# Kernel optimization log

Measured on AMD Instinct MI355X. Metric: run time of the kernel, lower is better.

The kernel has to match this reference:

```python
import jax, jax.numpy as jnp
import numpy as np

NUM_HIDDEN = 256   # per-head dim == model dim in this module
NUM_HEADS = 8
SEQ_LEN = 2048
BATCH = 4
D_K = 256          # self.d_k used for the softmax scale


def setup_inputs() -> dict:
    key = jax.random.key(0)
    ks = jax.random.split(key, 12)
    H, D = NUM_HEADS, NUM_HIDDEN
    init = lambda k, shape: (jax.random.normal(k, shape, dtype=jnp.float32) * 0.02)
    return {
        "query": jax.random.normal(ks[0], (BATCH, SEQ_LEN, D), dtype=jnp.float32),
        "key": jax.random.normal(ks[1], (BATCH, SEQ_LEN, D), dtype=jnp.float32),
        "values": jax.random.normal(ks[2], (BATCH, SEQ_LEN, D), dtype=jnp.float32),
        "Wq": init(ks[3], (H * D, D)), "bq": init(ks[4], (H * D,)),
        "Wk": init(ks[5], (H * D, D)), "bk": init(ks[6], (H * D,)),
        "Wv": init(ks[7], (H * D, D)), "bv": init(ks[8], (H * D,)),
        "Wo": init(ks[9], (D, H * D)), "bo": init(ks[10], (D,)),
    }


def reference(query, key, values, Wq, bq, Wk, bk, Wv, bv, Wo, bo):
    B, S, D = query.shape
    H = Wq.shape[0] // D
    # Linear projections to [B, S, H*D], then the module's raw reshape to [B, H, S, D]
    # (note: this is a plain view, NOT the usual split-heads transpose -> faithful to source)
    q = (jnp.einsum("bsd,ed->bse", query, Wq) + bq).reshape(B, H, S, D)
    k = (jnp.einsum("bsd,ed->bse", key, Wk) + bk).reshape(B, H, S, D)
    v = (jnp.einsum("bsd,ed->bse", values, Wv) + bv).reshape(B, H, S, D)
    # scores: [B, H, S, S], scaled by sqrt(d_k); default path applies no mask
    scores = jnp.einsum("bhqd,bhkd->bhqk", q, k) / jnp.sqrt(jnp.float32(D_K))
    attn = jax.nn.softmax(scores, axis=-1)
    # dropout in eval mode: identity
    out = jnp.einsum("bhqk,bhkd->bhqd", attn, v)            # [B, H, S, D]
    out = out.transpose(0, 2, 1, 3).reshape(B, S, H * D)    # [B, S, H*D]
    return jnp.einsum("bse,de->bsd", out, Wo) + bo          # [B, S, D]
```

## Files before the change

### kernel.cpp

```cpp
#include <hip/hip_runtime.h>
#include <hip/hip_bf16.h>
#include <stdint.h>

#define B_SZ 4
#define H_N 8
#define S_LEN 2048
#define D_HEAD 256
#define HD 2048

typedef __attribute__((ext_vector_type(8))) short bf16x8;
typedef __attribute__((ext_vector_type(4))) float f32x4;
typedef __attribute__((ext_vector_type(4))) uint32_t u32x4;
typedef __hip_bfloat16 bf16;

typedef __attribute__((address_space(1))) const void glob_cv;
typedef __attribute__((address_space(3))) void lds_v;

__device__ __forceinline__ short f2bf(float f) {
  bf16 h = __float2bfloat16(f);
  return *reinterpret_cast<short*>(&h);
}

__device__ __forceinline__ uint32_t cvtpk(float lo, float hi) {
  uint32_t r;
  asm volatile("v_cvt_pk_bf16_f32 %0, %1, %2" : "=v"(r) : "v"(lo), "v"(hi));
  return r;
}

__global__ __launch_bounds__(256) void cvt_all(
    const float* __restrict__ w0, bf16* __restrict__ o0,
    const float* __restrict__ w1, bf16* __restrict__ o1,
    const float* __restrict__ w2, bf16* __restrict__ o2,
    const float* __restrict__ w3, bf16* __restrict__ o3,
    const float* __restrict__ x0, bf16* __restrict__ y0,
    const float* __restrict__ x1, bf16* __restrict__ y1,
    const float* __restrict__ x2, bf16* __restrict__ y2) {
  int bid = blockIdx.x;
  const float* src; bf16* dst; int off;
  if (bid < 1024) {
    int k = bid >> 8; off = (bid & 255) * 2048;
    src = k == 0 ? w0 : k == 1 ? w1 : k == 2 ? w2 : w3;
    dst = k == 0 ? o0 : k == 1 ? o1 : k == 2 ? o2 : o3;
  } else {
    int j = bid - 1024; int k = j >> 10; off = (j & 1023) * 2048;
    src = k == 0 ? x0 : k == 1 ? x1 : x2;
    dst = k == 0 ? y0 : k == 1 ? y1 : y2;
  }
  int i = off + threadIdx.x * 8;
  float4 a = *(const float4*)(src + i);
  float4 b = *(const float4*)(src + i + 4);
  bf16x8 o;
  o[0] = f2bf(a.x); o[1] = f2bf(a.y); o[2] = f2bf(a.z); o[3] = f2bf(a.w);
  o[4] = f2bf(b.x); o[5] = f2bf(b.y); o[6] = f2bf(b.z); o[7] = f2bf(b.w);
  *reinterpret_cast<bf16x8*>(dst + i) = o;
}

__global__ __launch_bounds__(256, 2) void proj3(
    const bf16* __restrict__ A0, const bf16* __restrict__ A1, const bf16* __restrict__ A2,
    const bf16* __restrict__ B0, const bf16* __restrict__ B1, const bf16* __restrict__ B2,
    const float* __restrict__ c0, const float* __restrict__ c1, const float* __restrict__ c2,
    bf16* __restrict__ O0, bf16* __restrict__ O1, bf16* __restrict__ O2) {
  constexpr int HALF = 2 * 128 * 128;
  __shared__ __align__(16) char lds[2 * HALF];

  int which = blockIdx.y;
  const bf16* A = which == 0 ? A0 : which == 1 ? A1 : A2;
  const bf16* Bm = which == 0 ? B0 : which == 1 ? B1 : B2;
  const float* bias = which == 0 ? c0 : which == 1 ? c1 : c2;
  bf16* OutP = which == 0 ? O0 : which == 1 ? O1 : O2;
  float scale = which == 0 ? (1.0f / 16.0f) * 1.44269504f : 1.0f;

  int tid = threadIdx.x;
  int w = tid >> 6, l = tid & 63;
  int l15 = l & 15, lg = l >> 4;
  int wr = w >> 1, wc = w & 1;

  int bid = blockIdx.x;
  int wg = (bid & 7) * 128 + (bid >> 3);
  int mt = wg >> 4, nt = wg & 15;
  int m0 = mt * 128, n0 = nt * 128;

  const size_t K2 = 512;
  char* ldsp = (char*)lds;
  const char* Abase = (const char*)A + (size_t)m0 * K2;
  const char* Bbase = (const char*)Bm + (size_t)n0 * K2;

  auto ISSUE = [&](int buf, int kt) {
    const char* As = Abase + (size_t)kt * 128;
    const char* Bs = Bbase + (size_t)kt * 128;
    char* db = ldsp + buf * HALF;
#pragma unroll
    for (int i = 0; i < 4; ++i) {
      int c = tid + i * 256, row = c >> 3;
      __builtin_amdgcn_global_load_lds((glob_cv*)(As + (size_t)row * K2 + 16 * ((c & 7) ^ (row & 7))),
                                       (lds_v*)(db + c * 16), 16, 0, 0);
    }
#pragma unroll
    for (int i = 0; i < 4; ++i) {
      int c = tid + i * 256, row = c >> 3;
      __builtin_amdgcn_global_load_lds((glob_cv*)(Bs + (size_t)row * K2 + 16 * ((c & 7) ^ (row & 7))),
                                       (lds_v*)(db + 16384 + c * 16), 16, 0, 0);
    }
  };

  f32x4 acc[4][4];
#pragma unroll
  for (int mi = 0; mi < 4; ++mi)
#pragma unroll
    for (int ni = 0; ni < 4; ++ni) acc[mi][ni] = f32x4{0.f, 0.f, 0.f, 0.f};

  ISSUE(0, 0);
  for (int kt = 0; kt < 4; ++kt) {
    int cur = kt & 1;
    if (kt < 3) {
      ISSUE(cur ^ 1, kt + 1);
      asm volatile("s_waitcnt vmcnt(8)" ::: "memory");
    } else {
      asm volatile("s_waitcnt vmcnt(0)" ::: "memory");
    }
    __builtin_amdgcn_s_barrier();
    __builtin_amdgcn_sched_barrier(0);

    const char* bufc = ldsp + cur * HALF;
#pragma unroll
    for (int kb2 = 0; kb2 < 2; ++kb2) {
      int swz = 16 * ((kb2 * 4 + lg) ^ (l15 & 7));
      bf16x8 af[4], bfr[4];
#pragma unroll
      for (int mi = 0; mi < 4; ++mi)
        af[mi] = *(const bf16x8*)(bufc + (wr * 64 + mi * 16 + l15) * 128 + swz);
#pragma unroll
      for (int ni = 0; ni < 4; ++ni)
        bfr[ni] = *(const bf16x8*)(bufc + 16384 + (wc * 64 + ni * 16 + l15) * 128 + swz);
#pragma unroll
      for (int mi = 0; mi < 4; ++mi)
#pragma unroll
        for (int ni = 0; ni < 4; ++ni)
          acc[mi][ni] = __builtin_amdgcn_mfma_f32_16x16x32_bf16(af[mi], bfr[ni], acc[mi][ni], 0, 0, 0);
    }
    __builtin_amdgcn_sched_barrier(0);
    __builtin_amdgcn_s_barrier();
  }

  if (which == 2) {
    bf16* tp = (bf16*)lds;
#pragma unroll
    for (int ni = 0; ni < 4; ++ni) {
      int colL = wc * 64 + ni * 16 + l15;
      float bv = bias[n0 + colL];
#pragma unroll
      for (int mi = 0; mi < 4; ++mi) {
        short4 pk4;
        pk4.x = f2bf(acc[mi][ni][0] + bv);
        pk4.y = f2bf(acc[mi][ni][1] + bv);
        pk4.z = f2bf(acc[mi][ni][2] + bv);
        pk4.w = f2bf(acc[mi][ni][3] + bv);
        *(short4*)(tp + colL * 136 + wr * 64 + mi * 16 + lg * 4) = pk4;
      }
    }
    __syncthreads();
    int b = m0 >> 11, h = (m0 >> 8) & 7;
    int ehi = n0 >> 8, t0 = m0 & 255;
    bf16* vb = OutP + (size_t)(b * 8 + h) * D_HEAD * S_LEN;
#pragma unroll
    for (int p = 0; p < 8; ++p) {
      int colL = p * 16 + (tid >> 4);
      int d = (n0 & 255) + colL;
      int4 v = *(const int4*)(tp + colL * 136 + (tid & 15) * 8);
      *(int4*)(vb + (size_t)d * S_LEN + ehi * 256 + t0 + (tid & 15) * 8) = v;
    }
  } else {
#pragma unroll
    for (int ni = 0; ni < 4; ++ni) {
      int col = n0 + wc * 64 + ni * 16 + l15;
      float bv = bias[col];
#pragma unroll
      for (int mi = 0; mi < 4; ++mi) {
#pragma unroll
        for (int r = 0; r < 4; ++r) {
          float v = (acc[mi][ni][r] + bv) * scale;
          int row = m0 + wr * 64 + mi * 16 + lg * 4 + r;
          int b = row >> 11;
          int h = (row >> 8) & 7;
          int d = col & 255;
          size_t off;
          if (which == 1) {
            int jj = (col >> 8) * 256 + (row & 255);
            off = (((size_t)(b * 8 + h) * S_LEN) + jj) * D_HEAD + d;
          } else {
            int sp = ((row & 255) << 3) | (col >> 8);
            off = (((size_t)(b * 8 + h) * S_LEN) + sp) * D_HEAD + d;
          }
          OutP[off] = __float2bfloat16(v);
        }
      }
    }
  }
}

__global__ __launch_bounds__(256, 2) void out_gemm(const bf16* __restrict__ A,
                                                   const bf16* __restrict__ Bm,
                                                   const float* __restrict__ bias,
                                                   float* __restrict__ Out) {
  constexpr int HALF = 2 * 64 * 128;
  __shared__ __align__(16) char lds[2 * HALF];

  int tid = threadIdx.x;
  int w = tid >> 6, l = tid & 63;
  int l15 = l & 15, lg = l >> 4;
  int wr = w >> 1, wc = w & 1;

  int bid = blockIdx.x;
  int wg = (bid & 7) * 64 + (bid >> 3);
  int mt = wg >> 2, nt = wg & 3;
  int m0 = mt * 64, n0 = nt * 64;

  const size_t K2 = 4096;
  char* ldsp = (char*)lds;
  const char* Abase = (const char*)A + (size_t)m0 * K2;
  const char* Bbase = (const char*)Bm + (size_t)n0 * K2;

  auto ISSUE = [&](int buf, int kt) {
    const char* As = Abase + (size_t)kt * 128;
    const char* Bs = Bbase + (size_t)kt * 128;
    char* db = ldsp + buf * HALF;
#pragma unroll
    for (int i = 0; i < 2; ++i) {
      int c = tid + i * 256, row = c >> 3;
      __builtin_amdgcn_global_load_lds((glob_cv*)(As + (size_t)row * K2 + 16 * ((c & 7) ^ (row & 7))),
                                       (lds_v*)(db + c * 16), 16, 0, 0);
    }
#pragma unroll
    for (int i = 0; i < 2; ++i) {
      int c = tid + i * 256, row = c >> 3;
      __builtin_amdgcn_global_load_lds((glob_cv*)(Bs + (size_t)row * K2 + 16 * ((c & 7) ^ (row & 7))),
                                       (lds_v*)(db + 8192 + c * 16), 16, 0, 0);
    }
  };

  f32x4 acc[2][2];
#pragma unroll
  for (int mi = 0; mi < 2; ++mi)
#pragma unroll
    for (int ni = 0; ni < 2; ++ni) acc[mi][ni] = f32x4{0.f, 0.f, 0.f, 0.f};

  ISSUE(0, 0);
  for (int kt = 0; kt < 32; ++kt) {
    int cur = kt & 1;
    if (kt < 31) {
      ISSUE(cur ^ 1, kt + 1);
      asm volatile("s_waitcnt vmcnt(4)" ::: "memory");
    } else {
      asm volatile("s_waitcnt vmcnt(0)" ::: "memory");
    }
    __builtin_amdgcn_s_barrier();
    __builtin_amdgcn_sched_barrier(0);

    const char* bufc = ldsp + cur * HALF;
#pragma unroll
    for (int kb2 = 0; kb2 < 2; ++kb2) {
      int swz = 16 * ((kb2 * 4 + lg) ^ (l15 & 7));
      bf16x8 af[2], bfr[2];
#pragma unroll
      for (int mi = 0; mi < 2; ++mi)
        af[mi] = *(const bf16x8*)(bufc + (wr * 32 + mi * 16 + l15) * 128 + swz);
#pragma unroll
      for (int ni = 0; ni < 2; ++ni)
        bfr[ni] = *(const bf16x8*)(bufc + 8192 + (wc * 32 + ni * 16 + l15) * 128 + swz);
#pragma unroll
      for (int mi = 0; mi < 2; ++mi)
#pragma unroll
        for (int ni = 0; ni < 2; ++ni)
          acc[mi][ni] = __builtin_amdgcn_mfma_f32_16x16x32_bf16(af[mi], bfr[ni], acc[mi][ni], 0, 0, 0);
    }
    __builtin_amdgcn_sched_barrier(0);
    __builtin_amdgcn_s_barrier();
  }

#pragma unroll
  for (int ni = 0; ni < 2; ++ni) {
    int col = n0 + wc * 32 + ni * 16 + l15;
    float bv = bias[col];
#pragma unroll
    for (int mi = 0; mi < 2; ++mi)
#pragma unroll
      for (int r = 0; r < 4; ++r)
        Out[(size_t)(m0 + wr * 32 + mi * 16 + lg * 4 + r) * 256 + col] = acc[mi][ni][r] + bv;
  }
}

__global__ __launch_bounds__(256, 2) void attn_kernel(const bf16* __restrict__ Qp,
                                                      const bf16* __restrict__ Kp,
                                                      const bf16* __restrict__ Vt,
                                                      bf16* __restrict__ AL) {
  __shared__ __align__(16) bf16 KVs[2 * 16384];

  int tid = threadIdx.x;
  int w = tid >> 6, l = tid & 63;
  int l15 = l & 15, lg = l >> 4;
  int l31 = l & 31, hl = l >> 5;

  int bid = blockIdx.x;
  int xcd = bid & 7, j = bid >> 3;
  int bh = xcd + 8 * (j >> 4);
  int qt = j & 15;

  const bf16* Qb = Qp + (size_t)bh * S_LEN * D_HEAD;
  const bf16* Kb = Kp + (size_t)bh * S_LEN * D_HEAD;
  const bf16* Vb = Vt + (size_t)bh * (size_t)D_HEAD * S_LEN;

  int q0 = qt * 128 + w * 32;

  bf16x8 qf0[8], qf1[8];
#pragma unroll
  for (int kb = 0; kb < 8; ++kb) {
    qf0[kb] = *(const bf16x8*)(Qb + (size_t)(q0 + l15) * D_HEAD + kb * 32 + lg * 8);
    qf1[kb] = *(const bf16x8*)(Qb + (size_t)(q0 + 16 + l15) * D_HEAD + kb * 32 + lg * 8);
  }

  f32x4 acc0[16], acc1[16];
#pragma unroll
  for (int n = 0; n < 16; ++n) {
    acc0[n] = f32x4{0.f, 0.f, 0.f, 0.f};
    acc1[n] = f32x4{0.f, 0.f, 0.f, 0.f};
  }
  float lp0 = 0.f, lp1 = 0.f;

  int kvp = 2 * (l31 & 15) + (l31 >> 4);
  const char* pK = (const char*)Kb + (size_t)kvp * 512 + (size_t)(w * 256 + hl * 16);
  const char* pV = (const char*)Vb + (size_t)l * 4096 + (size_t)((w - 2) * 32);
  int dK = w * 8192 + l * 16;
  int dV = 16384 + (w - 2) * 8192 + l * 16;
  char* ldsBase = (char*)&KVs[0];

  auto ISSUE = [&](int buf) {
    char* bb = ldsBase + buf * 32768;
    if (w < 2) {
#pragma unroll
      for (int i = 0; i < 8; ++i)
        __builtin_amdgcn_global_load_lds((glob_cv*)(pK + i * 32),
                                         (lds_v*)(bb + dK + i * 1024), 16, 0, 0);
      pK += 32 * 512;
    } else {
#pragma unroll
      for (int i = 0; i < 8; ++i)
        __builtin_amdgcn_global_load_lds((glob_cv*)(pV + (i & 3) * 262144 + (i >> 2) * 16),
                                         (lds_v*)(bb + dV + (i & 3) * 1024 + (i >> 2) * 4096), 16, 0, 0);
      pV += 64;
    }
  };

  int krd = lg * 256 + l15 * 8;
  int vrd = 8192 + lg * 2048 + l15 * 8;

  ISSUE(0);

  for (int kt = 0; kt < 64; ++kt) {
    int cur = kt & 1;
    asm volatile("s_waitcnt vmcnt(0)" ::: "memory");
    __builtin_amdgcn_s_barrier();
    __builtin_amdgcn_sched_barrier(0);
    if (kt < 63) ISSUE(cur ^ 1);

    const bf16* bufp = &KVs[cur * 16384];

    f32x4 s00 = f32x4{0.f,0.f,0.f,0.f}, s01 = f32x4{0.f,0.f,0.f,0.f};
    f32x4 s10 = f32x4{0.f,0.f,0.f,0.f}, s11 = f32x4{0.f,0.f,0.f,0.f};
    __builtin_amdgcn_s_setprio(1);
#pragma unroll
    for (int kb = 0; kb < 8; ++kb) {
      bf16x8 kf0 = *(const bf16x8*)(bufp + krd + kb * 1024);
      bf16x8 kf1 = *(const bf16x8*)(bufp + krd + kb * 1024 + 128);
      s00 = __builtin_amdgcn_mfma_f32_16x16x32_bf16(kf0, qf0[kb], s00, 0, 0, 0);
      s01 = __builtin_amdgcn_mfma_f32_16x16x32_bf16(kf1, qf0[kb], s01, 0, 0, 0);
      s10 = __builtin_amdgcn_mfma_f32_16x16x32_bf16(kf0, qf1[kb], s10, 0, 0, 0);
      s11 = __builtin_amdgcn_mfma_f32_16x16x32_bf16(kf1, qf1[kb], s11, 0, 0, 0);
    }
    __builtin_amdgcn_s_setprio(0);

    float p00[4], p01[4], p10[4], p11[4];
#pragma unroll
    for (int r = 0; r < 4; ++r) {
      p00[r] = exp2f(s00[r]); p01[r] = exp2f(s01[r]);
      p10[r] = exp2f(s10[r]); p11[r] = exp2f(s11[r]);
    }
    lp0 += (p00[0] + p01[0]) + (p00[1] + p01[1]) + (p00[2] + p01[2]) + (p00[3] + p01[3]);
    lp1 += (p10[0] + p11[0]) + (p10[1] + p11[1]) + (p10[2] + p11[2]) + (p10[3] + p11[3]);

    union { u32x4 wq; bf16x8 v; } pu0, pu1;
    pu0.wq[0] = cvtpk(p00[0], p01[0]); pu0.wq[1] = cvtpk(p00[1], p01[1]);
    pu0.wq[2] = cvtpk(p00[2], p01[2]); pu0.wq[3] = cvtpk(p00[3], p01[3]);
    pu1.wq[0] = cvtpk(p10[0], p11[0]); pu1.wq[1] = cvtpk(p10[1], p11[1]);
    pu1.wq[2] = cvtpk(p10[2], p11[2]); pu1.wq[3] = cvtpk(p10[3], p11[3]);
    bf16x8 pa0 = pu0.v, pa1 = pu1.v;

    __builtin_amdgcn_s_setprio(1);
#pragma unroll
    for (int n = 0; n < 16; ++n) {
      bf16x8 vbf = *(const bf16x8*)(bufp + vrd + n * 128);
      acc0[n] = __builtin_amdgcn_mfma_f32_16x16x32_bf16(pa0, vbf, acc0[n], 0, 0, 0);
      acc1[n] = __builtin_amdgcn_mfma_f32_16x16x32_bf16(pa1, vbf, acc1[n], 0, 0, 0);
    }
    __builtin_amdgcn_s_setprio(0);
  }

  float t0 = lp0;
  t0 += __shfl_xor(t0, 16);
  t0 += __shfl_xor(t0, 32);
  float inv0 = 1.0f / t0;
  float t1 = lp1;
  t1 += __shfl_xor(t1, 16);
  t1 += __shfl_xor(t1, 32);
  float inv1 = 1.0f / t1;
  float i00 = __shfl(inv0, lg * 4 + 0), i01 = __shfl(inv0, lg * 4 + 1);
  float i02 = __shfl(inv0, lg * 4 + 2), i03 = __shfl(inv0, lg * 4 + 3);
  float i10 = __shfl(inv1, lg * 4 + 0), i11 = __shfl(inv1, lg * 4 + 1);
  float i12 = __shfl(inv1, lg * 4 + 2), i13 = __shfl(inv1, lg * 4 + 3);
  int b = bh >> 3, h = bh & 7;
#pragma unroll
  for (int r = 0; r < 4; ++r) {
    float v0 = r == 0 ? i00 : r == 1 ? i01 : r == 2 ? i02 : i03;
    float v1 = r == 0 ? i10 : r == 1 ? i11 : r == 2 ? i12 : i13;
    int qa = q0 + lg * 4 + r;
    int qb = qa + 16;
    bf16* orow0 = AL + ((size_t)b * S_LEN + qa) * HD + h * D_HEAD;
    bf16* orow1 = AL + ((size_t)b * S_LEN + qb) * HD + h * D_HEAD;
#pragma unroll
    for (int n = 0; n < 16; ++n) {
      orow0[n * 16 + l15] = __float2bfloat16(acc0[n][r] * v0);
      orow1[n * 16 + l15] = __float2bfloat16(acc1[n][r] * v1);
    }
  }
}

extern "C" void kernel_launch(void* const* d_in, const int* in_sizes, int n_in,
                              void* d_out, int out_size, void* d_ws, size_t ws_size,
                              hipStream_t stream) {
  (void)in_sizes; (void)n_in; (void)out_size; (void)ws_size;
  const float* query  = (const float*)d_in[0];
  const float* key    = (const float*)d_in[1];
  const float* values = (const float*)d_in[2];
  const float* Wq = (const float*)d_in[3];
  const float* bq = (const float*)d_in[4];
  const float* Wk = (const float*)d_in[5];
  const float* bk = (const float*)d_in[6];
  const float* Wv = (const float*)d_in[7];
  const float* bv = (const float*)d_in[8];
  const float* Wo = (const float*)d_in[9];
  const float* bo = (const float*)d_in[10];
  float* out = (float*)d_out;

  bf16* ws = (bf16*)d_ws;
  const size_t NP = (size_t)B_SZ * H_N * S_LEN * D_HEAD;
  const size_t NW = (size_t)HD * D_HEAD;
  const size_t NX = (size_t)B_SZ * S_LEN * D_HEAD;
  bf16* Qp  = ws;
  bf16* Kp  = Qp + NP;
  bf16* Vtp = Kp + NP;
  bf16* ALb = Vtp + NP;
  bf16* Wqb = ALb + NP;
  bf16* Wkb = Wqb + NW;
  bf16* Wvb = Wkb + NW;
  bf16* Wob = Wvb + NW;
  bf16* Xqb = ALb;
  bf16* Xkb = ALb + NX;
  bf16* Xvb = ALb + 2 * NX;

  cvt_all<<<4096, 256, 0, stream>>>(Wq, Wqb, Wk, Wkb, Wv, Wvb, Wo, Wob,
                                    query, Xqb, key, Xkb, values, Xvb);

  proj3<<<dim3(1024, 3), 256, 0, stream>>>(Xqb, Xkb, Xvb, Wqb, Wkb, Wvb,
                                           bq, bk, bv, Qp, Kp, Vtp);

  attn_kernel<<<512, 256, 0, stream>>>(Qp, Kp, Vtp, ALb);

  out_gemm<<<512, 256, 0, stream>>>(ALb, Wob, bo, out);
}
```

Baseline: 233.1 us.

## Software-pipeline attention loop: overlap PV of previous tile with QK of current

Restructures the attention inner loop so the P·V MFMAs for the previous key tile are issued right after the Q·K MFMAs of the current tile, and the exp/convert work follows them. The aim is to hide the softmax exp and packing latency behind matrix-core work. K stays double-buffered while V moves to a triple buffer so the previous tile's V remains valid. LDS per block grows from 64KB to 80KB, which may lower occupancy, and P fragments for the previous tile are kept live in registers across iterations.

```diff
diff --git a/kernel.cpp b/kernel.cpp
--- a/kernel.cpp
+++ b/kernel.cpp
@@ -293,7 +293,7 @@
                                                       const bf16* __restrict__ Kp,
                                                       const bf16* __restrict__ Vt,
                                                       bf16* __restrict__ AL) {
-  __shared__ __align__(16) bf16 KVs[2 * 16384];
+  __shared__ __align__(16) bf16 KVs[5 * 8192];
 
   int tid = threadIdx.x;
   int w = tid >> 6, l = tid & 63;
@@ -330,18 +330,19 @@
   const char* pK = (const char*)Kb + (size_t)kvp * 512 + (size_t)(w * 256 + hl * 16);
   const char* pV = (const char*)Vb + (size_t)l * 4096 + (size_t)((w - 2) * 32);
   int dK = w * 8192 + l * 16;
-  int dV = 16384 + (w - 2) * 8192 + l * 16;
+  int dV = (w - 2) * 8192 + l * 16;
   char* ldsBase = (char*)&KVs[0];
 
-  auto ISSUE = [&](int buf) {
-    char* bb = ldsBase + buf * 32768;
+  auto ISSUE = [&](int kbuf, int vbuf) {
     if (w < 2) {
+      char* bb = ldsBase + kbuf * 16384;
 #pragma unroll
       for (int i = 0; i < 8; ++i)
         __builtin_amdgcn_global_load_lds((glob_cv*)(pK + i * 32),
                                          (lds_v*)(bb + dK + i * 1024), 16, 0, 0);
       pK += 32 * 512;
     } else {
+      char* bb = ldsBase + 32768 + vbuf * 16384;
 #pragma unroll
       for (int i = 0; i < 8; ++i)
         __builtin_amdgcn_global_load_lds((glob_cv*)(pV + (i & 3) * 262144 + (i >> 2) * 16),
@@ -351,30 +352,44 @@
   };
 
   int krd = lg * 256 + l15 * 8;
-  int vrd = 8192 + lg * 2048 + l15 * 8;
-
-  ISSUE(0);
+  int vrd = lg * 2048 + l15 * 8;
+
+  ISSUE(0, 0);
+
+  bf16x8 paP0{}, paP1{};
+  int vPrev = 0, vThis = 0;
 
   for (int kt = 0; kt < 64; ++kt) {
-    int cur = kt & 1;
+    int kcur = kt & 1;
     asm volatile("s_waitcnt vmcnt(0)" ::: "memory");
     __builtin_amdgcn_s_barrier();
     __builtin_amdgcn_sched_barrier(0);
-    if (kt < 63) ISSUE(cur ^ 1);
-
-    const bf16* bufp = &KVs[cur * 16384];
-
+    int vNext = vThis + 1 == 3 ? 0 : vThis + 1;
+    if (kt < 63) ISSUE(kcur ^ 1, vNext);
+
+    const bf16* Kt = (const bf16*)ldsBase + kcur * 8192;
+    const bf16* Vp = (const bf16*)ldsBase + 16384 + vPrev * 8192;
+
+    __builtin_amdgcn_s_setprio(1);
     f32x4 s00 = f32x4{0.f,0.f,0.f,0.f}, s01 = f32x4{0.f,0.f,0.f,0.f};
     f32x4 s10 = f32x4{0.f,0.f,0.f,0.f}, s11 = f32x4{0.f,0.f,0.f,0.f};
-    __builtin_amdgcn_s_setprio(1);
 #pragma unroll
     for (int kb = 0; kb < 8; ++kb) {
-      bf16x8 kf0 = *(const bf16x8*)(bufp + krd + kb * 1024);
-      bf16x8 kf1 = *(const bf16x8*)(bufp + krd + kb * 1024 + 128);
+      bf16x8 kf0 = *(const bf16x8*)(Kt + krd + kb * 1024);
+      bf16x8 kf1 = *(const bf16x8*)(Kt + krd + kb * 1024 + 128);
       s00 = __builtin_amdgcn_mfma_f32_16x16x32_bf16(kf0, qf0[kb], s00, 0, 0, 0);
       s01 = __builtin_amdgcn_mfma_f32_16x16x32_bf16(kf1, qf0[kb], s01, 0, 0, 0);
       s10 = __builtin_amdgcn_mfma_f32_16x16x32_bf16(kf0, qf1[kb], s10, 0, 0, 0);
       s11 = __builtin_amdgcn_mfma_f32_16x16x32_bf16(kf1, qf1[kb], s11, 0, 0, 0);
+    }
+
+    if (kt > 0) {
+#pragma unroll
+      for (int n = 0; n < 16; ++n) {
+        bf16x8 vbf = *(const bf16x8*)(Vp + vrd + n * 128);
+        acc0[n] = __builtin_amdgcn_mfma_f32_16x16x32_bf16(paP0, vbf, acc0[n], 0, 0, 0);
+        acc1[n] = __builtin_amdgcn_mfma_f32_16x16x32_bf16(paP1, vbf, acc1[n], 0, 0, 0);
+      }
     }
     __builtin_amdgcn_s_setprio(0);
 
@@ -392,16 +407,19 @@
     pu0.wq[2] = cvtpk(p00[2], p01[2]); pu0.wq[3] = cvtpk(p00[3], p01[3]);
     pu1.wq[0] = cvtpk(p10[0], p11[0]); pu1.wq[1] = cvtpk(p10[1], p11[1]);
     pu1.wq[2] = cvtpk(p10[2], p11[2]); pu1.wq[3] = cvtpk(p10[3], p11[3]);
-    bf16x8 pa0 = pu0.v, pa1 = pu1.v;
-
-    __builtin_amdgcn_s_setprio(1);
+    paP0 = pu0.v; paP1 = pu1.v;
+
+    vPrev = vThis; vThis = vNext;
+  }
+
+  {
+    const bf16* Vp = (const bf16*)ldsBase + 16384 + vPrev * 8192;
 #pragma unroll
     for (int n = 0; n < 16; ++n) {
-      bf16x8 vbf = *(const bf16x8*)(bufp + vrd + n * 128);
-      acc0[n] = __builtin_amdgcn_mfma_f32_16x16x32_bf16(pa0, vbf, acc0[n], 0, 0, 0);
-      acc1[n] = __builtin_amdgcn_mfma_f32_16x16x32_bf16(pa1, vbf, acc1[n], 0, 0, 0);
-    }
-    __builtin_amdgcn_s_setprio(0);
+      bf16x8 vbf = *(const bf16x8*)(Vp + vrd + n * 128);
+      acc0[n] = __builtin_amdgcn_mfma_f32_16x16x32_bf16(paP0, vbf, acc0[n], 0, 0, 0);
+      acc1[n] = __builtin_amdgcn_mfma_f32_16x16x32_bf16(paP1, vbf, acc1[n], 0, 0, 0);
+    }
   }
 
   float t0 = lp0;
```

Measured after the change: 454.1 us. 94.8% more time.
